# Performance work log

Measured on AMD Instinct MI355X. Metric: run time of the kernel, lower is better.

The kernel has to match this reference:

```python
import jax, jax.numpy as jnp
import numpy as np

MODEL_DIM = 512
COND_DIM = 768
HEAD_DIM = 64
N_HEADS = 8


def setup_inputs() -> dict:
    key = jax.random.key(0)
    k1, k2, k3, k4, k5, k6 = jax.random.split(key, 6)
    inner = HEAD_DIM * N_HEADS
    x = jax.random.normal(k1, (16, 4096, MODEL_DIM), dtype=jnp.float32)
    cond = jax.random.normal(k2, (16, 77, COND_DIM), dtype=jnp.float32)
    # nn.Linear weights (out, in); apply as x @ W.T
    s = 0.02
    w_q = jax.random.normal(k3, (inner, MODEL_DIM), dtype=jnp.float32) * s
    w_k = jax.random.normal(k4, (inner, COND_DIM), dtype=jnp.float32) * s
    w_v = jax.random.normal(k5, (inner, COND_DIM), dtype=jnp.float32) * s
    w_o = jax.random.normal(k6, (MODEL_DIM, inner), dtype=jnp.float32) * s
    return {"x": x, "cond": cond, "w_q": w_q, "w_k": w_k, "w_v": w_v, "w_o": w_o}


def reference(x, cond, w_q, w_k, w_v, w_o):
    b, lq, _ = x.shape
    lk = cond.shape[1]
    q = (x @ w_q.T).reshape(b, lq, N_HEADS, HEAD_DIM)
    k = (cond @ w_k.T).reshape(b, lk, N_HEADS, HEAD_DIM)
    v = (cond @ w_v.T).reshape(b, lk, N_HEADS, HEAD_DIM)
    scale = HEAD_DIM ** -0.5
    attn = jnp.einsum('bihd,bjhd->bhij', q, k) * scale  # [b,h,lq,lk]
    attn = jax.nn.softmax(attn, axis=-1)
    out = jnp.einsum('bhij,bjhd->bihd', attn, v).reshape(b, lq, N_HEADS * HEAD_DIM)
    return out @ w_o.T
```

## Files before the change

kernel.cpp:

```cpp
#include <hip/hip_runtime.h>
#include <hip/hip_bf16.h>
#include <stdint.h>


typedef __bf16 bf16_t;
typedef __bf16 bf16x8 __attribute__((ext_vector_type(8)));
typedef float floatx4 __attribute__((ext_vector_type(4)));

#define MFMA16(a, b, c) __builtin_amdgcn_mfma_f32_16x16x32_bf16((a), (b), (c), 0, 0, 0)

__device__ __forceinline__ void gload_lds16(const bf16_t* g, bf16_t* l)
{
    __builtin_amdgcn_global_load_lds(
        (const __attribute__((address_space(1))) void*)g,
        (__attribute__((address_space(3))) void*)l, 16, 0, 0);
}

struct CvtArgs {
    const float* s[5];
    bf16_t* d[5];
};

__device__ __forceinline__ void cvt8(const float* in, bf16_t* out, long long i)
{
    floatx4 f0 = *(const floatx4*)(in + i * 8);
    floatx4 f1 = *(const floatx4*)(in + i * 8 + 4);
    bf16x8 v;
#pragma unroll
    for (int e = 0; e < 4; e++) { v[e] = (bf16_t)f0[e]; v[e + 4] = (bf16_t)f1[e]; }
    *(bf16x8*)(out + i * 8) = v;
}

__global__ __launch_bounds__(256) void cvt_all(
    const float* __restrict__ x, bf16_t* __restrict__ xb, long long n8x, CvtArgs c)
{
    if (blockIdx.y == 0) {
        for (long long i = (long long)blockIdx.x * 256 + threadIdx.x; i < n8x;
             i += (long long)2048 * 256)
            cvt8(x, xb, i);
    } else {
        int gid = blockIdx.x, seg, base;
        if      (gid <  462) { seg = 0; base = 0;   }
        else if (gid <  590) { seg = 1; base = 462; }
        else if (gid <  782) { seg = 2; base = 590; }
        else if (gid <  974) { seg = 3; base = 782; }
        else if (gid < 1102) { seg = 4; base = 974; }
        else return;
        long long i = (long long)(gid - base) * 256 + threadIdx.x;
        cvt8(c.s[seg], c.d[seg], i);
    }
}

template <bool CF32>
__global__ __launch_bounds__(256) void gemm_bt(
    const bf16_t* __restrict__ A, const bf16_t* __restrict__ B,
    void* __restrict__ Cv, int M, int N, int K)
{
    __shared__ bf16_t As[2 * 128 * 32];
    __shared__ bf16_t Bs[2 * 128 * 32];

    const int t = threadIdx.x;
    const int l = t & 63;
    const int w = t >> 6;
    const int wm = w >> 1, wn = w & 1;
    const int l15 = l & 15, l4 = l >> 4;

    const int nbx = gridDim.x;
    const int nwg = nbx * gridDim.y;
    int lid = blockIdx.y * nbx + blockIdx.x;
    if ((nwg & 7) == 0) {
        const int cpx = nwg >> 3;
        lid = (lid & 7) * cpx + (lid >> 3);
    }
    const int m0 = (lid / nbx) * 128, n0 = (lid % nbx) * 128;

    floatx4 acc[4][4] = {};

    const bf16_t* ag[4];
    const bf16_t* bg[4];
    bf16_t* al[4];
    bf16_t* bl[4];
#pragma unroll
    for (int i = 0; i < 4; i++) {
        int e = (i * 256 + t) * 8;
        int kk = e >> 12;
        int row = (e & 4095) >> 5;
        int col = kk * 32 + (e & 31);
        int ra = m0 + row; if (ra > M - 1) ra = M - 1;
        ag[i] = A + (size_t)ra * K + col;
        bg[i] = B + (size_t)(n0 + row) * K + col;
        al[i] = &As[e];
        bl[i] = &Bs[e];
    }

    for (int k0 = 0; k0 < K; k0 += 64) {
#pragma unroll
        for (int i = 0; i < 4; i++) {
            gload_lds16(ag[i] + k0, al[i]);
            gload_lds16(bg[i] + k0, bl[i]);
        }
        __syncthreads();

#pragma unroll
        for (int kk = 0; kk < 2; kk++) {
            bf16x8 af[4], bfr[4];
#pragma unroll
            for (int i = 0; i < 4; i++)
                af[i] = *(const bf16x8*)&As[kk * 4096 + (wm * 64 + i * 16 + l15) * 32 + l4 * 8];
#pragma unroll
            for (int j = 0; j < 4; j++)
                bfr[j] = *(const bf16x8*)&Bs[kk * 4096 + (wn * 64 + j * 16 + l15) * 32 + l4 * 8];
#pragma unroll
            for (int i = 0; i < 4; i++)
#pragma unroll
                for (int j = 0; j < 4; j++)
                    acc[i][j] = MFMA16(af[i], bfr[j], acc[i][j]);
        }
        __syncthreads();
    }

#pragma unroll
    for (int i = 0; i < 4; i++)
#pragma unroll
        for (int j = 0; j < 4; j++)
#pragma unroll
            for (int r = 0; r < 4; r++) {
                int row = m0 + wm * 64 + i * 16 + l4 * 4 + r;
                int col = n0 + wn * 64 + j * 16 + l15;
                if (row < M) {
                    if (CF32) ((float*)Cv)[(size_t)row * N + col] = acc[i][j][r];
                    else ((bf16_t*)Cv)[(size_t)row * N + col] = (bf16_t)acc[i][j][r];
                }
            }
}

#define LK 77
#define KVSTR 1024
#define KSTR 72
#define VSTR 104
#define JP 96

__global__ __launch_bounds__(256) void attn_fused(
    bf16_t* QO,
    const bf16_t* __restrict__ KVg)
{
    __shared__ bf16_t Ks[80 * KSTR];
    __shared__ bf16_t Vs[64 * VSTR];
    __shared__ bf16_t Ps[4 * 32 * VSTR];

    const int t = threadIdx.x;
    const int w = t >> 6, l = t & 63;
    const int l15 = l & 15, l4 = l >> 4;
    const int b = blockIdx.y >> 3, h = blockIdx.y & 7;
    const int q0 = blockIdx.x * 128;

    const bf16_t* qbase =
        QO + ((size_t)(b * 4096 + q0 + w * 32 + l15)) * 512 + h * 64 + l4 * 8;
    bf16x8 aq[2][2];
    aq[0][0] = *(const bf16x8*)qbase;
    aq[0][1] = *(const bf16x8*)(qbase + 32);
    aq[1][0] = *(const bf16x8*)(qbase + 16 * 512);
    aq[1][1] = *(const bf16x8*)(qbase + 16 * 512 + 32);

    const bf16_t* Kg = KVg;
    const bf16_t* Vg = KVg + 512;

    for (int idx = t; idx < LK * 8; idx += 256) {
        int j = idx >> 3, c = (idx & 7) * 8;
        *(uint4*)&Ks[j * KSTR + c] =
            *(const uint4*)&Kg[((size_t)(b * LK + j)) * KVSTR + h * 64 + c];
    }
    for (int idx = t; idx < 3 * KSTR; idx += 256)
        Ks[LK * KSTR + idx] = (bf16_t)0.0f;

    for (int u = t; u < LK * 8; u += 256) {
        int j = u >> 3, d0 = (u & 7) * 8;
        uint4 pk = *(const uint4*)&Vg[((size_t)(b * LK + j)) * KVSTR + h * 64 + d0];
        const bf16_t* pv = (const bf16_t*)&pk;
#pragma unroll
        for (int e = 0; e < 8; e++)
            Vs[(d0 + e) * VSTR + j] = pv[e];
    }
    for (int idx = t; idx < 64 * (JP - LK); idx += 256) {
        int d = idx / (JP - LK), j = LK + idx % (JP - LK);
        Vs[d * VSTR + j] = (bf16_t)0.0f;
    }
    __syncthreads();

    floatx4 s[2][5];
    __builtin_amdgcn_s_setprio(1);
#pragma unroll
    for (int n = 0; n < 5; n++) {
        bf16x8 b0 = *(const bf16x8*)&Ks[(n * 16 + l15) * KSTR + l4 * 8];
        bf16x8 b1 = *(const bf16x8*)&Ks[(n * 16 + l15) * KSTR + 32 + l4 * 8];
#pragma unroll
        for (int mi = 0; mi < 2; mi++) {
            floatx4 z = {0.f, 0.f, 0.f, 0.f};
            z = MFMA16(aq[mi][0], b0, z);
            z = MFMA16(aq[mi][1], b1, z);
            s[mi][n] = z;
        }
    }
    __builtin_amdgcn_s_setprio(0);

    const float scale = 0.125f;
    float p[2][5][4], linv[2][4];
#pragma unroll
    for (int mi = 0; mi < 2; mi++)
#pragma unroll
        for (int r = 0; r < 4; r++) {
            float smax = -1e30f;
#pragma unroll
            for (int n = 0; n < 5; n++) {
                float v = s[mi][n][r] * scale;
                if (n == 4 && (64 + l15) >= LK) v = -1e30f;
                p[mi][n][r] = v;
                smax = fmaxf(smax, v);
            }
#pragma unroll
            for (int off = 1; off < 16; off <<= 1)
                smax = fmaxf(smax, __shfl_xor(smax, off, 64));
            float sum = 0.f;
#pragma unroll
            for (int n = 0; n < 5; n++) {
                float e2 = __expf(p[mi][n][r] - smax);
                p[mi][n][r] = e2;
                sum += e2;
            }
#pragma unroll
            for (int off = 1; off < 16; off <<= 1)
                sum += __shfl_xor(sum, off, 64);
            linv[mi][r] = 1.0f / sum;
        }

    bf16_t* pw = Ps + w * 32 * VSTR;
#pragma unroll
    for (int mi = 0; mi < 2; mi++)
#pragma unroll
        for (int r = 0; r < 4; r++) {
            int row = mi * 16 + l4 * 4 + r;
#pragma unroll
            for (int n = 0; n < 5; n++)
                pw[row * VSTR + n * 16 + l15] = (bf16_t)(p[mi][n][r] * linv[mi][r]);
            pw[row * VSTR + 80 + l15] = (bf16_t)0.0f;
        }
    __syncthreads();

    bf16x8 ap[2][3];
#pragma unroll
    for (int mi = 0; mi < 2; mi++)
#pragma unroll
        for (int ks = 0; ks < 3; ks++)
            ap[mi][ks] = *(const bf16x8*)&pw[(mi * 16 + l15) * VSTR + ks * 32 + l4 * 8];
#pragma unroll
    for (int n2 = 0; n2 < 4; n2++) {
        bf16x8 bv[3];
#pragma unroll
        for (int ks = 0; ks < 3; ks++)
            bv[ks] = *(const bf16x8*)&Vs[(n2 * 16 + l15) * VSTR + ks * 32 + l4 * 8];
        floatx4 o[2];
        __builtin_amdgcn_s_setprio(1);
#pragma unroll
        for (int mi = 0; mi < 2; mi++) {
            floatx4 z = {0.f, 0.f, 0.f, 0.f};
#pragma unroll
            for (int ks = 0; ks < 3; ks++)
                z = MFMA16(ap[mi][ks], bv[ks], z);
            o[mi] = z;
        }
        __builtin_amdgcn_s_setprio(0);
#pragma unroll
        for (int mi = 0; mi < 2; mi++)
#pragma unroll
            for (int r = 0; r < 4; r++) {
                int q = q0 + w * 32 + mi * 16 + l4 * 4 + r;
                QO[((size_t)(b * 4096 + q)) * 512 + h * 64 + n2 * 16 + l15] =
                    (bf16_t)o[mi][r];
            }
    }
}

extern "C" void kernel_launch(void* const* d_in, const int* in_sizes, int n_in,
                              void* d_out, int out_size, void* d_ws, size_t ws_size,
                              hipStream_t stream)
{
    const float* x    = (const float*)d_in[0];
    const float* cond = (const float*)d_in[1];
    const float* w_q  = (const float*)d_in[2];
    const float* w_k  = (const float*)d_in[3];
    const float* w_v  = (const float*)d_in[4];
    const float* w_o  = (const float*)d_in[5];
    float* out = (float*)d_out;

    const int Mq  = 16 * 4096;
    const int Mkv = 16 * 77;

    bf16_t* Qb  = (bf16_t*)d_ws;
    bf16_t* KVb = Qb + (size_t)Mq * 512;
    bf16_t* Wob = KVb + (size_t)Mkv * 1024;

    bf16_t* Xb   = (bf16_t*)d_out;
    bf16_t* Cb   = Xb  + (size_t)Mq * 512;
    bf16_t* Wqb  = Cb  + (size_t)Mkv * 768;
    bf16_t* Wkvb = Wqb + (size_t)512 * 512;

    CvtArgs c;
    c.s[0] = cond; c.d[0] = Cb;
    c.s[1] = w_q;  c.d[1] = Wqb;
    c.s[2] = w_k;  c.d[2] = Wkvb;
    c.s[3] = w_v;  c.d[3] = Wkvb + (size_t)512 * 768;
    c.s[4] = w_o;  c.d[4] = Wob;
    cvt_all<<<dim3(2048, 2), 256, 0, stream>>>(x, Xb, (long long)Mq * 512 / 8, c);

    gemm_bt<false><<<dim3(4, Mq / 128), 256, 0, stream>>>(Xb, Wqb, Qb, Mq, 512, 512);
    gemm_bt<false><<<dim3(8, (Mkv + 127) / 128), 256, 0, stream>>>(Cb, Wkvb, KVb, Mkv, 1024, 768);

    attn_fused<<<dim3(32, 128), 256, 0, stream>>>(Qb, KVb);

    gemm_bt<true><<<dim3(4, Mq / 128), 256, 0, stream>>>(Qb, Wob, out, Mq, 512, 512);
}
```

Baseline: 403.3 us.

## Fuse fp32-to-bf16 conversion into GEMM loads and merge KV projection with weight prep

Removes the standalone conversion kernel. The Q-projection GEMM now reads fp32 x directly and converts it to bf16 while staging into LDS. A new prep kernel computes the KV projection straight from fp32 cond and weights while other blocks convert w_q and w_o, which cuts two launches and avoids writing and re-reading a bf16 copy of x (about 64MB of traffic). In exchange, the A-operand staging in the Q GEMM goes through registers with synchronous loads instead of asynchronous global-to-LDS loads, which may expose more load latency inside the main loop.

```diff
diff --git a/kernel.cpp b/kernel.cpp
--- a/kernel.cpp
+++ b/kernel.cpp
@@ -16,10 +16,15 @@
         (__attribute__((address_space(3))) void*)l, 16, 0, 0);
 }
 
-struct CvtArgs {
-    const float* s[5];
-    bf16_t* d[5];
-};
+__device__ __forceinline__ void stage_cvt8(const float* g, bf16_t* l)
+{
+    floatx4 f0 = *(const floatx4*)g;
+    floatx4 f1 = *(const floatx4*)(g + 4);
+    bf16x8 v;
+#pragma unroll
+    for (int e = 0; e < 4; e++) { v[e] = (bf16_t)f0[e]; v[e + 4] = (bf16_t)f1[e]; }
+    *(bf16x8*)l = v;
+}
 
 __device__ __forceinline__ void cvt8(const float* in, bf16_t* out, long long i)
 {
@@ -31,29 +36,9 @@
     *(bf16x8*)(out + i * 8) = v;
 }
 
-__global__ __launch_bounds__(256) void cvt_all(
-    const float* __restrict__ x, bf16_t* __restrict__ xb, long long n8x, CvtArgs c)
-{
-    if (blockIdx.y == 0) {
-        for (long long i = (long long)blockIdx.x * 256 + threadIdx.x; i < n8x;
-             i += (long long)2048 * 256)
-            cvt8(x, xb, i);
-    } else {
-        int gid = blockIdx.x, seg, base;
-        if      (gid <  462) { seg = 0; base = 0;   }
-        else if (gid <  590) { seg = 1; base = 462; }
-        else if (gid <  782) { seg = 2; base = 590; }
-        else if (gid <  974) { seg = 3; base = 782; }
-        else if (gid < 1102) { seg = 4; base = 974; }
-        else return;
-        long long i = (long long)(gid - base) * 256 + threadIdx.x;
-        cvt8(c.s[seg], c.d[seg], i);
-    }
-}
-
-template <bool CF32>
+template <bool AF32, bool CF32>
 __global__ __launch_bounds__(256) void gemm_bt(
-    const bf16_t* __restrict__ A, const bf16_t* __restrict__ B,
+    const void* __restrict__ Av, const bf16_t* __restrict__ B,
     void* __restrict__ Cv, int M, int N, int K)
 {
     __shared__ bf16_t As[2 * 128 * 32];
@@ -76,7 +61,8 @@
 
     floatx4 acc[4][4] = {};
 
-    const bf16_t* ag[4];
+    const float*  agf[4];
+    const bf16_t* agb[4];
     const bf16_t* bg[4];
     bf16_t* al[4];
     bf16_t* bl[4];
@@ -87,7 +73,8 @@
         int row = (e & 4095) >> 5;
         int col = kk * 32 + (e & 31);
         int ra = m0 + row; if (ra > M - 1) ra = M - 1;
-        ag[i] = A + (size_t)ra * K + col;
+        if (AF32) agf[i] = (const float*)Av + (size_t)ra * K + col;
+        else      agb[i] = (const bf16_t*)Av + (size_t)ra * K + col;
         bg[i] = B + (size_t)(n0 + row) * K + col;
         al[i] = &As[e];
         bl[i] = &Bs[e];
@@ -96,7 +83,8 @@
     for (int k0 = 0; k0 < K; k0 += 64) {
 #pragma unroll
         for (int i = 0; i < 4; i++) {
-            gload_lds16(ag[i] + k0, al[i]);
+            if (AF32) stage_cvt8(agf[i] + k0, al[i]);
+            else      gload_lds16(agb[i] + k0, al[i]);
             gload_lds16(bg[i] + k0, bl[i]);
         }
         __syncthreads();
@@ -134,6 +122,91 @@
             }
 }
 
+__global__ __launch_bounds__(256) void prep(
+    const float* __restrict__ cond, const float* __restrict__ w_k,
+    const float* __restrict__ w_v, const float* __restrict__ w_q,
+    const float* __restrict__ w_o, bf16_t* __restrict__ KVb,
+    bf16_t* __restrict__ Wqb, bf16_t* __restrict__ Wob)
+{
+    __shared__ bf16_t As[2 * 128 * 32];
+    __shared__ bf16_t Bs[2 * 128 * 32];
+
+    const int bid = blockIdx.x;
+    const int t = threadIdx.x;
+
+    if (bid >= 80) {
+        if (bid < 208) cvt8(w_q, Wqb, (long long)(bid - 80) * 256 + t);
+        else           cvt8(w_o, Wob, (long long)(bid - 208) * 256 + t);
+        return;
+    }
+
+    const int l = t & 63;
+    const int w = t >> 6;
+    const int wm = w >> 1, wn = w & 1;
+    const int l15 = l & 15, l4 = l >> 4;
+    const int m0 = (bid >> 3) * 128, n0 = (bid & 7) * 128;
+    const int M = 1232, K = 768;
+
+    floatx4 acc[4][4] = {};
+
+    const float* ag[4];
+    const float* bg[4];
+    bf16_t* al[4];
+    bf16_t* bl[4];
+#pragma unroll
+    for (int i = 0; i < 4; i++) {
+        int e = (i * 256 + t) * 8;
+        int kk = e >> 12;
+        int row = (e & 4095) >> 5;
+        int col = kk * 32 + (e & 31);
+        int ra = m0 + row; if (ra > M - 1) ra = M - 1;
+        ag[i] = cond + (size_t)ra * K + col;
+        int rb = n0 + row;
+        bg[i] = (rb < 512 ? w_k + (size_t)rb * K
+                          : w_v + (size_t)(rb - 512) * K) + col;
+        al[i] = &As[e];
+        bl[i] = &Bs[e];
+    }
+
+    for (int k0 = 0; k0 < K; k0 += 64) {
+#pragma unroll
+        for (int i = 0; i < 4; i++) {
+            stage_cvt8(ag[i] + k0, al[i]);
+            stage_cvt8(bg[i] + k0, bl[i]);
+        }
+        __syncthreads();
+
+#pragma unroll
+        for (int kk = 0; kk < 2; kk++) {
+            bf16x8 af[4], bfr[4];
+#pragma unroll
+            for (int i = 0; i < 4; i++)
+                af[i] = *(const bf16x8*)&As[kk * 4096 + (wm * 64 + i * 16 + l15) * 32 + l4 * 8];
+#pragma unroll
+            for (int j = 0; j < 4; j++)
+                bfr[j] = *(const bf16x8*)&Bs[kk * 4096 + (wn * 64 + j * 16 + l15) * 32 + l4 * 8];
+#pragma unroll
+            for (int i = 0; i < 4; i++)
+#pragma unroll
+                for (int j = 0; j < 4; j++)
+                    acc[i][j] = MFMA16(af[i], bfr[j], acc[i][j]);
+        }
+        __syncthreads();
+    }
+
+#pragma unroll
+    for (int i = 0; i < 4; i++)
+#pragma unroll
+        for (int j = 0; j < 4; j++)
+#pragma unroll
+            for (int r = 0; r < 4; r++) {
+                int row = m0 + wm * 64 + i * 16 + l4 * 4 + r;
+                int col = n0 + wn * 64 + j * 16 + l15;
+                if (row < M)
+                    KVb[(size_t)row * 1024 + col] = (bf16_t)acc[i][j][r];
+            }
+}
+
 #define LK 77
 #define KVSTR 1024
 #define KSTR 72
@@ -296,26 +369,15 @@
     const int Mkv = 16 * 77;
 
     bf16_t* Qb  = (bf16_t*)d_ws;
-    bf16_t* KVb = Qb + (size_t)Mq * 512;
-    bf16_t* Wob = KVb + (size_t)Mkv * 1024;
-
-    bf16_t* Xb   = (bf16_t*)d_out;
-    bf16_t* Cb   = Xb  + (size_t)Mq * 512;
-    bf16_t* Wqb  = Cb  + (size_t)Mkv * 768;
-    bf16_t* Wkvb = Wqb + (size_t)512 * 512;
-
-    CvtArgs c;
-    c.s[0] = cond; c.d[0] = Cb;
-    c.s[1] = w_q;  c.d[1] = Wqb;
-    c.s[2] = w_k;  c.d[2] = Wkvb;
-    c.s[3] = w_v;  c.d[3] = Wkvb + (size_t)512 * 768;
-    c.s[4] = w_o;  c.d[4] = Wob;
-    cvt_all<<<dim3(2048, 2), 256, 0, stream>>>(x, Xb, (long long)Mq * 512 / 8, c);
-
-    gemm_bt<false><<<dim3(4, Mq / 128), 256, 0, stream>>>(Xb, Wqb, Qb, Mq, 512, 512);
-    gemm_bt<false><<<dim3(8, (Mkv + 127) / 128), 256, 0, stream>>>(Cb, Wkvb, KVb, Mkv, 1024, 768);
+    bf16_t* KVb = Qb  + (size_t)Mq * 512;
+    bf16_t* Wqb = KVb + (size_t)Mkv * 1024;
+    bf16_t* Wob = Wqb + (size_t)512 * 512;
+
+    prep<<<dim3(336), 256, 0, stream>>>(cond, w_k, w_v, w_q, w_o, KVb, Wqb, Wob);
+
+    gemm_bt<true, false><<<dim3(4, Mq / 128), 256, 0, stream>>>(x, Wqb, Qb, Mq, 512, 512);
 
     attn_fused<<<dim3(32, 128), 256, 0, stream>>>(Qb, KVb);
 
-    gemm_bt<true><<<dim3(4, Mq / 128), 256, 0, stream>>>(Qb, Wob, out, Mq, 512, 512);
-}
+    gemm_bt<false, true><<<dim3(4, Mq / 128), 256, 0, stream>>>(Qb, Wob, out, Mq, 512, 512);
+}
```

Measured after the change: 398.6 us. No clear change (-1.2%).
